# Optimization experiments

Hardware: AMD Instinct MI355X
Metric: run time of the kernel (lower is better)

Reference implementation:

```python
import jax, jax.numpy as jnp
import numpy as np

N = 50000      # nodes
E = 500000     # edges (before self-loops)
IN = 128       # input_channels
HID = 64       # hidden_channels
HEADS = 4
OUT = 10       # output_channels
G = 64         # number of graphs in batch


def setup_inputs() -> dict:
    key = jax.random.key(0)
    ks = jax.random.split(key, 12)
    x = jax.random.normal(ks[0], (N, IN), jnp.float32)
    edge_index = jax.random.randint(ks[1], (2, E), 0, N, jnp.int32)
    edge_weight = jax.random.uniform(ks[2], (E,), jnp.float32)
    batch = jnp.sort(jax.random.randint(ks[3], (N,), 0, G, jnp.int32))
    # GATConv layer 1: heads=4, concat=True
    W1 = jax.random.normal(ks[4], (HEADS * HID, IN), jnp.float32) / np.sqrt(IN)
    att_src1 = jax.random.normal(ks[5], (1, HEADS, HID), jnp.float32) / np.sqrt(HID)
    att_dst1 = jax.random.normal(ks[6], (1, HEADS, HID), jnp.float32) / np.sqrt(HID)
    b1 = jnp.zeros((HEADS * HID,), jnp.float32)
    # GATConv layer 2: heads=1, concat=False
    W2 = jax.random.normal(ks[7], (OUT, HEADS * HID), jnp.float32) / np.sqrt(HEADS * HID)
    att_src2 = jax.random.normal(ks[8], (1, 1, OUT), jnp.float32) / np.sqrt(OUT)
    att_dst2 = jax.random.normal(ks[9], (1, 1, OUT), jnp.float32) / np.sqrt(OUT)
    b2 = jnp.zeros((OUT,), jnp.float32)
    return {"x": x, "edge_index": edge_index, "edge_weight": edge_weight, "batch": batch,
            "W1": W1, "att_src1": att_src1, "att_dst1": att_dst1, "b1": b1,
            "W2": W2, "att_src2": att_src2, "att_dst2": att_dst2, "b2": b2}


def _gat_layer(x, src, dst, W, a_src, a_dst, heads, ch, n):
    # x: [n, in] -> h: [n, heads, ch]
    h = (x @ W.T).reshape(n, heads, ch)
    alpha_s = (h * a_src).sum(-1)  # [n, heads]
    alpha_d = (h * a_dst).sum(-1)
    e = jax.nn.leaky_relu(alpha_s[src] + alpha_d[dst], 0.2)  # [E', heads]
    # segment softmax over incoming edges of each destination node
    emax = jax.ops.segment_max(e, dst, num_segments=n)
    emax = jnp.where(jnp.isfinite(emax), emax, 0.0)
    ee = jnp.exp(e - emax[dst])
    denom = jax.ops.segment_sum(ee, dst, num_segments=n)
    alpha = ee / (denom[dst] + 1e-16)
    # weighted scatter-add of source features
    return jax.ops.segment_sum(alpha[:, :, None] * h[src], dst, num_segments=n)


def reference(x, edge_index, edge_weight, batch, W1, att_src1, att_dst1, b1,
              W2, att_src2, att_dst2, b2):
    # eval mode: dropout inactive; edge_weight is ignored by GATConv (as in source)
    n = x.shape[0]
    loops = jnp.arange(n, dtype=edge_index.dtype)  # PyG add_self_loops=True
    src = jnp.concatenate([edge_index[0], loops])
    dst = jnp.concatenate([edge_index[1], loops])
    h1 = _gat_layer(x, src, dst, W1, att_src1, att_dst1, HEADS, HID, n)
    h1 = jax.nn.elu(h1.reshape(n, HEADS * HID) + b1)
    h2 = _gat_layer(h1, src, dst, W2, att_src2, att_dst2, 1, OUT, n)[:, 0, :] + b2
    # global mean pool over graphs
    counts = jax.ops.segment_sum(jnp.ones((n,), h2.dtype), batch, num_segments=G)
    pooled = jax.ops.segment_sum(h2, batch, num_segments=G) / jnp.maximum(counts, 1.0)[:, None]
    return jax.nn.log_softmax(pooled, axis=1)
```

## Files before the change

### kernel.cpp

```cpp
#include <hip/hip_runtime.h>
#include <hip/hip_bf16.h>
#include <math.h>

#define NN 50000
#define EE 500000
#define ETOT (EE + NN)
#define NG 64

typedef __attribute__((ext_vector_type(8))) short short8v;
typedef __attribute__((ext_vector_type(4))) float float4v;
typedef __attribute__((ext_vector_type(2))) float float2v;

__device__ __forceinline__ float bf2f(unsigned short u) {
    unsigned int v = ((unsigned int)u) << 16;
    return __builtin_bit_cast(float, v);
}
__device__ __forceinline__ unsigned short f2bf(float f) {
    __hip_bfloat16 h = __float2bfloat16(f);
    return *(unsigned short*)&h;
}

__global__ void k_setup(uint4* __restrict__ zp, int n16, int zB,
                        const float* __restrict__ W1, unsigned short* __restrict__ wb,
                        const float* __restrict__ x, unsigned short* __restrict__ xb) {
    int b = blockIdx.x;
    if (b < zB) {
        int t = b * 256 + threadIdx.x;
        if (t < n16) zp[t] = make_uint4(0, 0, 0, 0);
    } else if (b < zB + 128) {
        int t = (b - zB) * 256 + threadIdx.x;
        wb[t] = f2bf(W1[t]);
    } else {
        int t = (b - zB - 128) * 256 + threadIdx.x;
        if (t < NN * 128 / 8) {
            float4 a = *(const float4*)&x[(size_t)t * 8];
            float4 c = *(const float4*)&x[(size_t)t * 8 + 4];
            float f[8] = {a.x, a.y, a.z, a.w, c.x, c.y, c.z, c.w};
            short8v vh;
#pragma unroll
            for (int j = 0; j < 8; ++j) vh[j] = (short)f2bf(f[j]);
            *(short8v*)&xb[(size_t)t * 8] = vh;
        }
    }
}

__global__ void k_hist(const int* __restrict__ ei, const int* __restrict__ batch,
                       int* __restrict__ counts, int* __restrict__ ord,
                       int* __restrict__ gcount) {
    int t = blockIdx.x * 256 + threadIdx.x;
    if (t < ETOT) {
        int dst = (t < EE) ? ei[EE + t] : (t - EE);
        ord[t] = atomicAdd(counts + dst, 1);
    }
    if (t < NN) {
        int g = batch[t];
        int g0 = __shfl(g, 0);
        bool same = (g == g0);
        unsigned long long m = __ballot(same);
        if (same) {
            if ((threadIdx.x & 63) == (__ffsll((long long)m) - 1))
                atomicAdd(gcount + g0, (int)__popcll(m));
        } else {
            atomicAdd(gcount + g, 1);
        }
    }
}

__global__ void k_scan(const int* __restrict__ counts, int* __restrict__ indptr) {
    __shared__ int wsum[16];
    __shared__ int carry_s;
    int tid = threadIdx.x;
    int lane = tid & 63;
    int w = tid >> 6;
    int4 v[13];
#pragma unroll
    for (int c = 0; c < 13; ++c) {
        int i = c * 4096 + tid * 4;
        if (i + 3 < NN) {
            v[c] = *(const int4*)&counts[i];
        } else {
            v[c] = make_int4(0, 0, 0, 0);
            if (i < NN) v[c].x = counts[i];
            if (i + 1 < NN) v[c].y = counts[i + 1];
            if (i + 2 < NN) v[c].z = counts[i + 2];
        }
    }
    if (tid == 0) carry_s = 0;
    __syncthreads();
#pragma unroll
    for (int c = 0; c < 13; ++c) {
        int i = c * 4096 + tid * 4;
        int v0 = v[c].x, v1 = v[c].y, v2 = v[c].z, v3 = v[c].w;
        int tot = v0 + v1 + v2 + v3;
        int s = tot;
#pragma unroll
        for (int off = 1; off < 64; off <<= 1) {
            int u = __shfl_up(s, off);
            if (lane >= off) s += u;
        }
        if (lane == 63) wsum[w] = s;
        __syncthreads();
        if (w == 0) {
            int t2 = (lane < 16) ? wsum[lane] : 0;
#pragma unroll
            for (int off = 1; off < 16; off <<= 1) {
                int u = __shfl_up(t2, off);
                if (lane >= off) t2 += u;
            }
            if (lane < 16) wsum[lane] = t2;
        }
        __syncthreads();
        int wpre = (w == 0) ? 0 : wsum[w - 1];
        int incl = s + wpre;
        int carry = carry_s;
        int e = carry + incl - tot;
        if (i < NN)     indptr[i] = e;
        if (i + 1 < NN) indptr[i + 1] = e + v0;
        if (i + 2 < NN) indptr[i + 2] = e + v0 + v1;
        if (i + 3 < NN) indptr[i + 3] = e + v0 + v1 + v2;
        __syncthreads();
        if (tid == 1023) carry_s = carry + incl;
        __syncthreads();
    }
    if (tid == 0) indptr[NN] = carry_s;
}

__global__ __launch_bounds__(256) void k_gemm1(const unsigned short* __restrict__ xb,
                                               const unsigned short* __restrict__ wb,
                                               const float* __restrict__ att_s,
                                               const float* __restrict__ att_d,
                                               unsigned char* __restrict__ h1f8,
                                               float* __restrict__ alpha_s,
                                               float* __restrict__ alpha_d) {
    int w = threadIdx.x >> 6;
    int l = threadIdx.x & 63;
    int bm0 = blockIdx.x * 32;
    int i16 = l & 15;
    int kb = (l >> 4) * 8;
    int colb = w * 64;

    short8v a[2][4];
#pragma unroll
    for (int mi = 0; mi < 2; ++mi) {
        int r = bm0 + mi * 16 + i16;
#pragma unroll
        for (int k = 0; k < 4; ++k) {
            if (r < NN) a[mi][k] = *(const short8v*)&xb[(size_t)r * 128 + k * 32 + kb];
            else        a[mi][k] = (short8v){0,0,0,0,0,0,0,0};
        }
    }

    float4v acc[2][4];
#pragma unroll
    for (int mi = 0; mi < 2; ++mi)
#pragma unroll
        for (int ni = 0; ni < 4; ++ni)
            acc[mi][ni] = (float4v){0.f, 0.f, 0.f, 0.f};

#pragma unroll
    for (int k = 0; k < 4; ++k) {
#pragma unroll
        for (int ni = 0; ni < 4; ++ni) {
            short8v b = *(const short8v*)&wb[(size_t)(colb + ni * 16 + i16) * 128 + k * 32 + kb];
            acc[0][ni] = __builtin_amdgcn_mfma_f32_16x16x32_bf16(a[0][k], b, acc[0][ni], 0, 0, 0);
            acc[1][ni] = __builtin_amdgcn_mfma_f32_16x16x32_bf16(a[1][k], b, acc[1][ni], 0, 0, 0);
        }
    }

    int drb = (l >> 4) * 4;
    int dc = l & 15;
    float asw[4], adw[4];
#pragma unroll
    for (int ni = 0; ni < 4; ++ni) {
        asw[ni] = att_s[colb + ni * 16 + dc];
        adw[ni] = att_d[colb + ni * 16 + dc];
    }
#pragma unroll
    for (int mi = 0; mi < 2; ++mi) {
#pragma unroll
        for (int r = 0; r < 4; ++r) {
            int row = bm0 + mi * 16 + drb + r;
            float v0 = acc[mi][0][r], v1 = acc[mi][1][r];
            float v2 = acc[mi][2][r], v3 = acc[mi][3][r];
            float s = v0 * asw[0] + v1 * asw[1] + v2 * asw[2] + v3 * asw[3];
            float d = v0 * adw[0] + v1 * adw[1] + v2 * adw[2] + v3 * adw[3];
            unsigned int packed = __builtin_amdgcn_cvt_pk_fp8_f32(v0, v1, 0u, false);
            packed = __builtin_amdgcn_cvt_pk_fp8_f32(v2, v3, packed, true);
            if (row < NN)
                *(unsigned int*)&h1f8[((unsigned)row << 8) + (unsigned)(colb + (dc << 2))] = packed;
#pragma unroll
            for (int m = 8; m >= 1; m >>= 1) {
                s += __shfl_xor(s, m);
                d += __shfl_xor(d, m);
            }
            if (dc == 0 && row < NN) {
                alpha_s[row * 4 + w] = s;
                alpha_d[row * 4 + w] = d;
            }
        }
    }
}

__global__ void k_fill(const int* __restrict__ ei, const int* __restrict__ indptr,
                       const int* __restrict__ ord,
                       const float* __restrict__ als, const float* __restrict__ ald,
                       uint4* __restrict__ edges, int* __restrict__ srcs) {
    int t = blockIdx.x * 256 + threadIdx.x;
    if (t >= ETOT) return;
    int src = (t < EE) ? ei[t] : (t - EE);
    int dst = (t < EE) ? ei[EE + t] : (t - EE);
    int p = indptr[dst] + ord[t];
    float4 as = *(const float4*)&als[src * 4];
    float4 ad = *(const float4*)&ald[dst * 4];
    float e0 = as.x + ad.x, e1 = as.y + ad.y, e2 = as.z + ad.z, e3 = as.w + ad.w;
    e0 = e0 > 0.f ? e0 : 0.2f * e0;
    e1 = e1 > 0.f ? e1 : 0.2f * e1;
    e2 = e2 > 0.f ? e2 : 0.2f * e2;
    e3 = e3 > 0.f ? e3 : 0.2f * e3;
    unsigned int ee01 = (unsigned int)f2bf(__expf(e0)) | ((unsigned int)f2bf(__expf(e1)) << 16);
    unsigned int ee23 = (unsigned int)f2bf(__expf(e2)) | ((unsigned int)f2bf(__expf(e3)) << 16);
    edges[p] = make_uint4((unsigned int)src, ee01, ee23, (unsigned int)dst);
    srcs[p] = src;
}

__global__ void k_gather1(const int* __restrict__ indptr, const uint4* __restrict__ edges,
                          const unsigned char* __restrict__ h1f8, const float* __restrict__ b1,
                          const float* __restrict__ W2, const float* __restrict__ as2v,
                          const float* __restrict__ ad2v, float* __restrict__ h2lin,
                          float* __restrict__ als2, float* __restrict__ ald2) {
    int wid = (blockIdx.x * 256 + threadIdx.x) >> 6;
    int l = threadIdx.x & 63;
    if (wid >= NN) return;
    int p0 = __builtin_amdgcn_readfirstlane(indptr[wid]);
    int p1 = __builtin_amdgcn_readfirstlane(indptr[wid + 1]);
    int last = p1 - 1;
    int head = l >> 4;
    unsigned sel = (head == 0) ? 0x01000C0Cu : (head == 1) ? 0x03020C0Cu
                 : (head == 2) ? 0x05040C0Cu : 0x07060C0Cu;
    unsigned lofs = (unsigned)(l << 2);
    float2v accA = {0.f, 0.f}, accB = {0.f, 0.f};
    float dsum = 0.f;
    for (int p = p0; p < p1; p += 8) {
        uint4 e[8];
#pragma unroll
        for (int j = 0; j < 8; ++j) {
            int idx = p + j;
            e[j] = edges[idx < p1 ? idx : last];
        }
        unsigned int hv[8];
#pragma unroll
        for (int j = 0; j < 8; ++j)
            hv[j] = *(const unsigned int*)(h1f8 + (((unsigned)e[j].x << 8) | lofs));
#pragma unroll
        for (int j = 0; j < 8; ++j) {
#if __has_builtin(__builtin_amdgcn_perm)
            unsigned wu = __builtin_amdgcn_perm(e[j].z, e[j].y, sel);
#else
            unsigned packed = (head & 2) ? e[j].z : e[j].y;
            unsigned wu = (head & 1) ? (packed & 0xffff0000u) : (packed << 16);
#endif
            float wgt = __builtin_bit_cast(float, wu);
            wgt = (p + j < p1) ? wgt : 0.f;
            float2v lo = __builtin_amdgcn_cvt_pk_f32_fp8(hv[j], false);
            float2v hi = __builtin_amdgcn_cvt_pk_f32_fp8(hv[j], true);
            float2v w2 = {wgt, wgt};
            accA += w2 * lo;
            accB += w2 * hi;
            dsum += wgt;
        }
    }
    float inv = 1.0f / dsum;
    int cbase = head * 64 + (l & 15);
    float o0 = accA[0] * inv + b1[cbase];
    float o1 = accA[1] * inv + b1[cbase + 16];
    float o2 = accB[0] * inv + b1[cbase + 32];
    float o3 = accB[1] * inv + b1[cbase + 48];
    o0 = o0 > 0.f ? o0 : (__expf(o0) - 1.0f);
    o1 = o1 > 0.f ? o1 : (__expf(o1) - 1.0f);
    o2 = o2 > 0.f ? o2 : (__expf(o2) - 1.0f);
    o3 = o3 > 0.f ? o3 : (__expf(o3) - 1.0f);
    float t[10];
#pragma unroll
    for (int o = 0; o < 10; ++o) {
        const float* wr = &W2[o * 256 + cbase];
        t[o] = o0 * wr[0] + o1 * wr[16] + o2 * wr[32] + o3 * wr[48];
    }
#pragma unroll
    for (int m = 32; m > 0; m >>= 1) {
#pragma unroll
        for (int o = 0; o < 10; ++o) t[o] += __shfl_xor(t[o], m);
    }
    if (l == 0) {
        float as = 0.f, ad = 0.f;
#pragma unroll
        for (int o = 0; o < 10; ++o) {
            h2lin[(size_t)wid * 16 + o] = t[o];
            as += t[o] * as2v[o];
            ad += t[o] * ad2v[o];
        }
        als2[wid] = as;
        ald2[wid] = ad;
    }
}

__global__ void k_g2pool(const int* __restrict__ indptr, const int* __restrict__ srcs,
                         const float* __restrict__ als2, const float* __restrict__ ald2,
                         const float* __restrict__ h2lin, const float* __restrict__ b2,
                         const int* __restrict__ batch, float* __restrict__ pooled) {
    int wave = (blockIdx.x * 256 + threadIdx.x) >> 6;
    int lane = threadIdx.x & 63;
    int grp = lane >> 4, c = lane & 15;
    int node = wave * 4 + grp;
    float acc = 0.f;
    int g = -1;
    if (node < NN) {
        int p0 = indptr[node], p1 = indptr[node + 1];
        int last = p1 - 1;
        float ad2n = ald2[node];
        float dsum = 0.f;
        for (int p = p0; p < p1; p += 4) {
            int i1 = p + 1, i2 = p + 2, i3 = p + 3;
            unsigned s0 = (unsigned)srcs[p];
            unsigned s1 = (unsigned)srcs[i1 < p1 ? i1 : last];
            unsigned s2 = (unsigned)srcs[i2 < p1 ? i2 : last];
            unsigned s3 = (unsigned)srcs[i3 < p1 ? i3 : last];
            float v0 = als2[s0] + ad2n;
            float v1 = als2[s1] + ad2n;
            float v2 = als2[s2] + ad2n;
            float v3 = als2[s3] + ad2n;
            float h0 = 0.f, h1_ = 0.f, h2 = 0.f, h3 = 0.f;
            if (c < 10) {
                h0 = h2lin[(s0 << 4) + (unsigned)c];
                h1_ = h2lin[(s1 << 4) + (unsigned)c];
                h2 = h2lin[(s2 << 4) + (unsigned)c];
                h3 = h2lin[(s3 << 4) + (unsigned)c];
            }
            v0 = v0 > 0.f ? v0 : 0.2f * v0;
            v1 = v1 > 0.f ? v1 : 0.2f * v1;
            v2 = v2 > 0.f ? v2 : 0.2f * v2;
            v3 = v3 > 0.f ? v3 : 0.2f * v3;
            float w0 = __expf(v0);
            float w1 = (i1 < p1) ? __expf(v1) : 0.f;
            float w2 = (i2 < p1) ? __expf(v2) : 0.f;
            float w3 = (i3 < p1) ? __expf(v3) : 0.f;
            dsum += (w0 + w1) + (w2 + w3);
            acc += w0 * h0 + w1 * h1_ + w2 * h2 + w3 * h3;
        }
        if (c < 10) acc = acc / dsum + b2[c];
        else acc = 0.f;
        g = batch[node];
    }
    int g0 = __shfl(g, 0);
    bool uni = __all((node >= NN) || (g == g0));
    if (uni) {
        if (g0 >= 0) {
            acc += __shfl_xor(acc, 16);
            acc += __shfl_xor(acc, 32);
            if (grp == 0 && c < 10)
                atomicAdd(pooled + g0 * 10 + c, acc);
        }
    } else if (node < NN && c < 10) {
        atomicAdd(pooled + g * 10 + c, acc);
    }
}

__global__ void k_final(const float* __restrict__ pooled, const int* __restrict__ gcount,
                        float* __restrict__ out) {
    int g = threadIdx.x;
    if (g >= NG) return;
    float c = fmaxf((float)gcount[g], 1.0f);
    float m[10];
    float mx = -1e30f;
#pragma unroll
    for (int i = 0; i < 10; ++i) {
        m[i] = pooled[g * 10 + i] / c;
        mx = fmaxf(mx, m[i]);
    }
    float s = 0.f;
#pragma unroll
    for (int i = 0; i < 10; ++i) s += expf(m[i] - mx);
    float lse = mx + logf(s);
#pragma unroll
    for (int i = 0; i < 10; ++i) out[g * 10 + i] = m[i] - lse;
}

extern "C" void kernel_launch(void* const* d_in, const int* in_sizes, int n_in,
                              void* d_out, int out_size, void* d_ws, size_t ws_size,
                              hipStream_t stream) {
    const float* x   = (const float*)d_in[0];
    const int*   ei  = (const int*)d_in[1];
    const int*   bat = (const int*)d_in[3];
    const float* W1  = (const float*)d_in[4];
    const float* as1 = (const float*)d_in[5];
    const float* ad1 = (const float*)d_in[6];
    const float* b1  = (const float*)d_in[7];
    const float* W2  = (const float*)d_in[8];
    const float* as2 = (const float*)d_in[9];
    const float* ad2 = (const float*)d_in[10];
    const float* b2  = (const float*)d_in[11];
    float* out = (float*)d_out;

    char* ws = (char*)d_ws;
    size_t off = 0;
    auto alloc = [&](size_t bytes) -> size_t {
        size_t o = off;
        off = (off + bytes + 255) & ~(size_t)255;
        return o;
    };
    size_t o_counts = alloc((size_t)NN * 4);
    size_t o_pooled = alloc((size_t)NG * 10 * 4);
    size_t o_gcount = alloc((size_t)NG * 4);
    size_t zero_bytes = off;
    size_t o_ord    = alloc((size_t)ETOT * 4);
    size_t o_indptr = alloc((size_t)(NN + 1) * 4);
    size_t o_edges  = alloc((size_t)ETOT * 16);
    size_t o_srcs   = alloc((size_t)ETOT * 4);
    size_t o_h1f8   = alloc((size_t)NN * 256);
    size_t o_als1   = alloc((size_t)NN * 4 * 4);
    size_t o_ald1   = alloc((size_t)NN * 4 * 4);
    size_t o_h2lin  = alloc((size_t)NN * 16 * 4);
    size_t o_als2   = alloc((size_t)NN * 4);
    size_t o_ald2   = alloc((size_t)NN * 4);
    size_t o_wb     = alloc((size_t)256 * 128 * 2);
    size_t o_xb     = alloc((size_t)NN * 128 * 2);
    (void)ws_size;

    int*   counts = (int*)(ws + o_counts);
    float* pooled = (float*)(ws + o_pooled);
    int*   gcount = (int*)(ws + o_gcount);
    int*   ord    = (int*)(ws + o_ord);
    int*   indptr = (int*)(ws + o_indptr);
    uint4* edges  = (uint4*)(ws + o_edges);
    int*   srcs   = (int*)(ws + o_srcs);
    unsigned char*  h1f8 = (unsigned char*)(ws + o_h1f8);
    float* als1   = (float*)(ws + o_als1);
    float* ald1   = (float*)(ws + o_ald1);
    float* h2lin  = (float*)(ws + o_h2lin);
    float* als2   = (float*)(ws + o_als2);
    float* ald2   = (float*)(ws + o_ald2);
    unsigned short* wb = (unsigned short*)(ws + o_wb);
    unsigned short* xb = (unsigned short*)(ws + o_xb);

    int n16 = (int)(zero_bytes / 16);
    int zB = (n16 + 255) / 256;
    int xB = (NN * 128 / 8 + 255) / 256;
    int gE = (ETOT + 255) / 256;
    int gW = (NN + 3) / 4;

    k_setup<<<zB + 128 + xB, 256, 0, stream>>>((uint4*)ws, n16, zB, W1, wb, x, xb);
    k_hist<<<gE, 256, 0, stream>>>(ei, bat, counts, ord, gcount);
    k_scan<<<1, 1024, 0, stream>>>(counts, indptr);
    k_gemm1<<<(NN + 31) / 32, 256, 0, stream>>>(xb, wb, as1, ad1, h1f8, als1, ald1);
    k_fill<<<gE, 256, 0, stream>>>(ei, indptr, ord, als1, ald1, edges, srcs);
    k_gather1<<<gW, 256, 0, stream>>>(indptr, edges, h1f8, b1, W2, as2, ad2,
                                      h2lin, als2, ald2);
    k_g2pool<<<gW, 256, 0, stream>>>(indptr, srcs, als2, ald2, h2lin, b2, bat, pooled);
    k_final<<<1, 64, 0, stream>>>(pooled, gcount, out);
    (void)n_in; (void)in_sizes; (void)out_size;
}
```

Measured before the change: 172.5 us.

## Merge launches: co-schedule hist with conversion, scan with GEMM, fold final into pool

The kernel sequence is restructured to cut the number of dependent launches. The histogram now runs inside the bf16 conversion kernel, while the zeroing moves to its own small kernel. The single-block scan is rewritten for 256 threads with per-thread serial chunks and runs as block 0 of the GEMM kernel. The final log-softmax is folded into the pooling kernel through a last-block-done atomic counter. This removes launch gaps and idle time on the serial scan, at the cost of an extra atomic per block and a scan that no longer runs at full width.

```diff
diff --git a/kernel.cpp b/kernel.cpp
--- a/kernel.cpp
+++ b/kernel.cpp
@@ -20,18 +20,22 @@
     return *(unsigned short*)&h;
 }
 
-__global__ void k_setup(uint4* __restrict__ zp, int n16, int zB,
-                        const float* __restrict__ W1, unsigned short* __restrict__ wb,
-                        const float* __restrict__ x, unsigned short* __restrict__ xb) {
+__global__ void k_zero(uint4* __restrict__ p, int n16) {
+    int t = blockIdx.x * 256 + threadIdx.x;
+    if (t < n16) p[t] = make_uint4(0, 0, 0, 0);
+}
+
+__global__ void k_phase0(const float* __restrict__ W1, unsigned short* __restrict__ wb,
+                         const float* __restrict__ x, unsigned short* __restrict__ xb,
+                         int xB, const int* __restrict__ ei, const int* __restrict__ batch,
+                         int* __restrict__ counts, int* __restrict__ ord,
+                         int* __restrict__ gcount) {
     int b = blockIdx.x;
-    if (b < zB) {
+    if (b < 128) {
         int t = b * 256 + threadIdx.x;
-        if (t < n16) zp[t] = make_uint4(0, 0, 0, 0);
-    } else if (b < zB + 128) {
-        int t = (b - zB) * 256 + threadIdx.x;
         wb[t] = f2bf(W1[t]);
-    } else {
-        int t = (b - zB - 128) * 256 + threadIdx.x;
+    } else if (b < 128 + xB) {
+        int t = (b - 128) * 256 + threadIdx.x;
         if (t < NN * 128 / 8) {
             float4 a = *(const float4*)&x[(size_t)t * 8];
             float4 c = *(const float4*)&x[(size_t)t * 8 + 4];
@@ -41,100 +45,91 @@
             for (int j = 0; j < 8; ++j) vh[j] = (short)f2bf(f[j]);
             *(short8v*)&xb[(size_t)t * 8] = vh;
         }
-    }
-}
-
-__global__ void k_hist(const int* __restrict__ ei, const int* __restrict__ batch,
-                       int* __restrict__ counts, int* __restrict__ ord,
-                       int* __restrict__ gcount) {
-    int t = blockIdx.x * 256 + threadIdx.x;
-    if (t < ETOT) {
-        int dst = (t < EE) ? ei[EE + t] : (t - EE);
-        ord[t] = atomicAdd(counts + dst, 1);
-    }
-    if (t < NN) {
-        int g = batch[t];
-        int g0 = __shfl(g, 0);
-        bool same = (g == g0);
-        unsigned long long m = __ballot(same);
-        if (same) {
-            if ((threadIdx.x & 63) == (__ffsll((long long)m) - 1))
-                atomicAdd(gcount + g0, (int)__popcll(m));
+    } else {
+        int t = (b - 128 - xB) * 256 + threadIdx.x;
+        if (t < ETOT) {
+            int dst = (t < EE) ? ei[EE + t] : (t - EE);
+            ord[t] = atomicAdd(counts + dst, 1);
+        }
+        if (t < NN) {
+            int g = batch[t];
+            int g0 = __shfl(g, 0);
+            bool same = (g == g0);
+            unsigned long long m = __ballot(same);
+            if (same) {
+                if ((threadIdx.x & 63) == (__ffsll((long long)m) - 1))
+                    atomicAdd(gcount + g0, (int)__popcll(m));
+            } else {
+                atomicAdd(gcount + g, 1);
+            }
+        }
+    }
+}
+
+__device__ void scan_body(const int* __restrict__ counts, int* __restrict__ indptr) {
+    __shared__ int wsums[4];
+    int t = threadIdx.x;
+    int lane = t & 63, wv = t >> 6;
+    int base = t * 196;
+    int S = 0;
+    for (int j = 0; j < 196; j += 4) {
+        int i = base + j;
+        if (i + 3 < NN) {
+            int4 v = *(const int4*)&counts[i];
+            S += (v.x + v.y) + (v.z + v.w);
         } else {
-            atomicAdd(gcount + g, 1);
-        }
-    }
-}
-
-__global__ void k_scan(const int* __restrict__ counts, int* __restrict__ indptr) {
-    __shared__ int wsum[16];
-    __shared__ int carry_s;
-    int tid = threadIdx.x;
-    int lane = tid & 63;
-    int w = tid >> 6;
-    int4 v[13];
-#pragma unroll
-    for (int c = 0; c < 13; ++c) {
-        int i = c * 4096 + tid * 4;
+            if (i < NN) S += counts[i];
+            if (i + 1 < NN) S += counts[i + 1];
+            if (i + 2 < NN) S += counts[i + 2];
+            if (i + 3 < NN) S += counts[i + 3];
+        }
+    }
+    int s = S;
+#pragma unroll
+    for (int off = 1; off < 64; off <<= 1) {
+        int u = __shfl_up(s, off);
+        if (lane >= off) s += u;
+    }
+    if (lane == 63) wsums[wv] = s;
+    __syncthreads();
+    int wpre = 0;
+#pragma unroll
+    for (int k = 0; k < 4; ++k) wpre += (k < wv) ? wsums[k] : 0;
+    int run = wpre + s - S;
+    for (int j = 0; j < 196; j += 4) {
+        int i = base + j;
         if (i + 3 < NN) {
-            v[c] = *(const int4*)&counts[i];
+            int4 v = *(const int4*)&counts[i];
+            int4 o;
+            o.x = run; o.y = run + v.x; o.z = o.y + v.y; o.w = o.z + v.z;
+            run = o.w + v.w;
+            *(int4*)&indptr[i] = o;
         } else {
-            v[c] = make_int4(0, 0, 0, 0);
-            if (i < NN) v[c].x = counts[i];
-            if (i + 1 < NN) v[c].y = counts[i + 1];
-            if (i + 2 < NN) v[c].z = counts[i + 2];
-        }
-    }
-    if (tid == 0) carry_s = 0;
-    __syncthreads();
-#pragma unroll
-    for (int c = 0; c < 13; ++c) {
-        int i = c * 4096 + tid * 4;
-        int v0 = v[c].x, v1 = v[c].y, v2 = v[c].z, v3 = v[c].w;
-        int tot = v0 + v1 + v2 + v3;
-        int s = tot;
-#pragma unroll
-        for (int off = 1; off < 64; off <<= 1) {
-            int u = __shfl_up(s, off);
-            if (lane >= off) s += u;
-        }
-        if (lane == 63) wsum[w] = s;
-        __syncthreads();
-        if (w == 0) {
-            int t2 = (lane < 16) ? wsum[lane] : 0;
-#pragma unroll
-            for (int off = 1; off < 16; off <<= 1) {
-                int u = __shfl_up(t2, off);
-                if (lane >= off) t2 += u;
+            for (int q = 0; q < 4; ++q) {
+                int ii = i + q;
+                if (ii < NN) { indptr[ii] = run; run += counts[ii]; }
             }
-            if (lane < 16) wsum[lane] = t2;
-        }
-        __syncthreads();
-        int wpre = (w == 0) ? 0 : wsum[w - 1];
-        int incl = s + wpre;
-        int carry = carry_s;
-        int e = carry + incl - tot;
-        if (i < NN)     indptr[i] = e;
-        if (i + 1 < NN) indptr[i + 1] = e + v0;
-        if (i + 2 < NN) indptr[i + 2] = e + v0 + v1;
-        if (i + 3 < NN) indptr[i + 3] = e + v0 + v1 + v2;
-        __syncthreads();
-        if (tid == 1023) carry_s = carry + incl;
-        __syncthreads();
-    }
-    if (tid == 0) indptr[NN] = carry_s;
-}
-
-__global__ __launch_bounds__(256) void k_gemm1(const unsigned short* __restrict__ xb,
-                                               const unsigned short* __restrict__ wb,
-                                               const float* __restrict__ att_s,
-                                               const float* __restrict__ att_d,
-                                               unsigned char* __restrict__ h1f8,
-                                               float* __restrict__ alpha_s,
-                                               float* __restrict__ alpha_d) {
+        }
+    }
+    if (t == 255) indptr[NN] = run;
+}
+
+__global__ __launch_bounds__(256) void k_phase1(const int* __restrict__ counts,
+                                                int* __restrict__ indptr,
+                                                const unsigned short* __restrict__ xb,
+                                                const unsigned short* __restrict__ wb,
+                                                const float* __restrict__ att_s,
+                                                const float* __restrict__ att_d,
+                                                unsigned char* __restrict__ h1f8,
+                                                float* __restrict__ alpha_s,
+                                                float* __restrict__ alpha_d) {
+    if (blockIdx.x == 0) {
+        scan_body(counts, indptr);
+        return;
+    }
     int w = threadIdx.x >> 6;
     int l = threadIdx.x & 63;
-    int bm0 = blockIdx.x * 32;
+    int bm0 = (blockIdx.x - 1) * 32;
     int i16 = l & 15;
     int kb = (l >> 4) * 8;
     int colb = w * 64;
@@ -306,7 +301,9 @@
 __global__ void k_g2pool(const int* __restrict__ indptr, const int* __restrict__ srcs,
                          const float* __restrict__ als2, const float* __restrict__ ald2,
                          const float* __restrict__ h2lin, const float* __restrict__ b2,
-                         const int* __restrict__ batch, float* __restrict__ pooled) {
+                         const int* __restrict__ batch, float* __restrict__ pooled,
+                         const int* __restrict__ gcount, int* __restrict__ done,
+                         float* __restrict__ out) {
     int wave = (blockIdx.x * 256 + threadIdx.x) >> 6;
     int lane = threadIdx.x & 63;
     int grp = lane >> 4, c = lane & 15;
@@ -362,26 +359,30 @@
     } else if (node < NN && c < 10) {
         atomicAdd(pooled + g * 10 + c, acc);
     }
-}
-
-__global__ void k_final(const float* __restrict__ pooled, const int* __restrict__ gcount,
-                        float* __restrict__ out) {
-    int g = threadIdx.x;
-    if (g >= NG) return;
-    float c = fmaxf((float)gcount[g], 1.0f);
-    float m[10];
-    float mx = -1e30f;
-#pragma unroll
-    for (int i = 0; i < 10; ++i) {
-        m[i] = pooled[g * 10 + i] / c;
-        mx = fmaxf(mx, m[i]);
-    }
-    float s = 0.f;
-#pragma unroll
-    for (int i = 0; i < 10; ++i) s += expf(m[i] - mx);
-    float lse = mx + logf(s);
-#pragma unroll
-    for (int i = 0; i < 10; ++i) out[g * 10 + i] = m[i] - lse;
+    __shared__ int lastflag;
+    if (threadIdx.x == 0) {
+        __threadfence();
+        int old = atomicAdd(done, 1);
+        lastflag = (old == (int)gridDim.x - 1);
+    }
+    __syncthreads();
+    if (lastflag && threadIdx.x < NG) {
+        int gg = threadIdx.x;
+        float cnt = fmaxf((float)atomicAdd((int*)gcount + gg, 0), 1.0f);
+        float m[10];
+        float mx = -1e30f;
+#pragma unroll
+        for (int i = 0; i < 10; ++i) {
+            m[i] = atomicAdd(pooled + gg * 10 + i, 0.0f) / cnt;
+            mx = fmaxf(mx, m[i]);
+        }
+        float s = 0.f;
+#pragma unroll
+        for (int i = 0; i < 10; ++i) s += expf(m[i] - mx);
+        float lse = mx + logf(s);
+#pragma unroll
+        for (int i = 0; i < 10; ++i) out[gg * 10 + i] = m[i] - lse;
+    }
 }
 
 extern "C" void kernel_launch(void* const* d_in, const int* in_sizes, int n_in,
@@ -410,6 +411,7 @@
     size_t o_counts = alloc((size_t)NN * 4);
     size_t o_pooled = alloc((size_t)NG * 10 * 4);
     size_t o_gcount = alloc((size_t)NG * 4);
+    size_t o_done   = alloc(256);
     size_t zero_bytes = off;
     size_t o_ord    = alloc((size_t)ETOT * 4);
     size_t o_indptr = alloc((size_t)(NN + 1) * 4);
@@ -428,6 +430,7 @@
     int*   counts = (int*)(ws + o_counts);
     float* pooled = (float*)(ws + o_pooled);
     int*   gcount = (int*)(ws + o_gcount);
+    int*   done   = (int*)(ws + o_done);
     int*   ord    = (int*)(ws + o_ord);
     int*   indptr = (int*)(ws + o_indptr);
     uint4* edges  = (uint4*)(ws + o_edges);
@@ -447,14 +450,15 @@
     int gE = (ETOT + 255) / 256;
     int gW = (NN + 3) / 4;
 
-    k_setup<<<zB + 128 + xB, 256, 0, stream>>>((uint4*)ws, n16, zB, W1, wb, x, xb);
-    k_hist<<<gE, 256, 0, stream>>>(ei, bat, counts, ord, gcount);
-    k_scan<<<1, 1024, 0, stream>>>(counts, indptr);
-    k_gemm1<<<(NN + 31) / 32, 256, 0, stream>>>(xb, wb, as1, ad1, h1f8, als1, ald1);
+    k_zero<<<zB, 256, 0, stream>>>((uint4*)ws, n16);
+    k_phase0<<<128 + xB + gE, 256, 0, stream>>>(W1, wb, x, xb, xB, ei, bat,
+                                                counts, ord, gcount);
+    k_phase1<<<1 + (NN + 31) / 32, 256, 0, stream>>>(counts, indptr, xb, wb,
+                                                     as1, ad1, h1f8, als1, ald1);
     k_fill<<<gE, 256, 0, stream>>>(ei, indptr, ord, als1, ald1, edges, srcs);
     k_gather1<<<gW, 256, 0, stream>>>(indptr, edges, h1f8, b1, W2, as2, ad2,
                                       h2lin, als2, ald2);
-    k_g2pool<<<gW, 256, 0, stream>>>(indptr, srcs, als2, ald2, h2lin, b2, bat, pooled);
-    k_final<<<1, 64, 0, stream>>>(pooled, gcount, out);
+    k_g2pool<<<gW, 256, 0, stream>>>(indptr, srcs, als2, ald2, h2lin, b2, bat,
+                                     pooled, gcount, done, out);
     (void)n_in; (void)in_sizes; (void)out_size;
 }
```

Result: slower. 368.7 us (+113.8%).
